# Kernel optimization log

Measured on AMD Instinct MI355X. Metric: run time of the kernel, lower is better.

Reference implementation:

```python
import jax, jax.numpy as jnp
import numpy as np

EMB = 256
HID = 1024
N_TRACKS = 4096
SEQ = 9
SCALE = 4.0


def setup_inputs() -> dict:
    key = jax.random.key(0)
    ks = jax.random.split(key, 12)

    def init(k, shape, fan_in):
        b = 1.0 / np.sqrt(fan_in)
        return jax.random.uniform(k, shape, jnp.float32, -b, b)

    return {
        "observed": jax.random.normal(ks[0], (SEQ, N_TRACKS, 2), jnp.float32),
        "emb_w": init(ks[1], (EMB - 2, 2), 2),
        "emb_b": init(ks[2], (EMB - 2,), 2),
        "enc_wih": init(ks[3], (4 * HID, EMB), HID),
        "enc_whh": init(ks[4], (4 * HID, HID), HID),
        "enc_b": init(ks[5], (4 * HID,), HID),
        "dec_wih": init(ks[6], (4 * HID, EMB), HID),
        "dec_whh": init(ks[7], (4 * HID, HID), HID),
        "dec_b": init(ks[8], (4 * HID,), HID),
        "h2n_w": init(ks[9], (5, HID), HID),
        "h2n_b": init(ks[10], (5,), HID),
        "n_predict": 12,
    }


def _forward(observed, emb_w, emb_b, enc_wih, enc_whh, enc_b,
             dec_wih, dec_whh, dec_b, h2n_w, h2n_b, n_predict):
    n = observed.shape[1]
    H = enc_whh.shape[1]
    E = enc_wih.shape[1]

    def cell(x, h, c, wih, whh, b):
        # PyTorch LSTMCell gate order: i, f, g, o
        g = x @ wih.T + h @ whh.T + b
        i, f, gg, o = jnp.split(g, 4, axis=-1)
        c = jax.nn.sigmoid(f) * c + jax.nn.sigmoid(i) * jnp.tanh(gg)
        h = jax.nn.sigmoid(o) * jnp.tanh(c)
        return h, c

    def embed(v):
        # Linear(2, E-2) -> ReLU, then 2 zero tag channels
        e = jax.nn.relu((v * SCALE) @ emb_w.T + emb_b)
        return jnp.concatenate([e, jnp.zeros((v.shape[0], 2), e.dtype)], axis=1)

    def h2n(h):
        raw = h @ h2n_w.T + h2n_b
        sig = 0.01 + 0.2 * jax.nn.sigmoid(raw[:, 2:4])  # sigma1, sigma2
        rho = 0.7 * jax.nn.sigmoid(raw[:, 4:5])          # rho
        return jnp.concatenate([raw[:, :2], sig, rho], axis=1)

    def step(params, h, c, obs1, obs2):
        wih, whh, b = params
        mask = ~(jnp.isnan(obs1[:, 0]) | jnp.isnan(obs2[:, 0]))  # [N]
        x = embed(obs2 - obs1)
        h2, c2 = cell(x, h, c, wih, whh, b)
        nrm = h2n(h2)
        m = mask[:, None]
        h = jnp.where(m, h2, h)
        c = jnp.where(m, c2, c)
        normal = jnp.where(m, nrm, jnp.nan)
        pos = obs2 + normal[:, :2]
        return h, c, normal, pos

    h = jnp.zeros((n, H), observed.dtype)
    c = jnp.zeros((n, H), observed.dtype)

    # encoder start tag
    tag_enc = jnp.zeros((n, E), observed.dtype).at[:, -2].set(1.0)
    h, c = cell(tag_enc, h, c, enc_wih, enc_whh, enc_b)

    enc_p = (enc_wih, enc_whh, enc_b)

    def enc_scan(carry, obs_pair):
        h, c = carry
        o1, o2 = obs_pair
        h, c, normal, pos = step(enc_p, h, c, o1, o2)
        return (h, c), (normal, pos)

    (h, c), (enc_normals, enc_positions) = jax.lax.scan(
        enc_scan, (h, c), (observed[:-1], observed[1:]))

    # decoder start tag
    tag_dec = jnp.zeros((n, E), observed.dtype).at[:, -1].set(1.0)
    h, c = cell(tag_dec, h, c, dec_wih, dec_whh, dec_b)

    dec_p = (dec_wih, dec_whh, dec_b)
    p1, p2 = enc_positions[-2], enc_positions[-1]

    def dec_scan(carry, _):
        h, c, p1, p2 = carry
        o1 = jax.lax.stop_gradient(p1)  # .detach() in torch
        o2 = jax.lax.stop_gradient(p2)
        h, c, normal, pos = step(dec_p, h, c, o1, o2)
        return (h, c, p2, pos), (normal, pos)

    _, (dec_normals, dec_positions) = jax.lax.scan(
        dec_scan, (h, c, p1, p2), None, length=n_predict - 1)

    rel_pred_scene = jnp.concatenate([enc_normals, dec_normals], axis=0)
    pred_scene = jnp.concatenate([enc_positions, dec_positions], axis=0)
    return rel_pred_scene, pred_scene


def reference(observed, emb_w, emb_b, enc_wih, enc_whh, enc_b,
              dec_wih, dec_whh, dec_b, h2n_w, h2n_b, n_predict):
    return _forward(observed, emb_w, emb_b, enc_wih, enc_whh, enc_b,
                    dec_wih, dec_whh, dec_b, h2n_w, h2n_b, n_predict)
```

## Files before the change

### kernel.cpp

```cpp
#include <hip/hip_runtime.h>
#include <stdint.h>

#define NTRK 4096
#define HIDN 1024
#define EMBN 256
#define KTOT 1280
#define NOUT 19

typedef __attribute__((ext_vector_type(8))) short short8;
typedef __attribute__((ext_vector_type(4))) float f32x4;

typedef __attribute__((address_space(1))) const void GV;
typedef __attribute__((address_space(3))) void LV;

__device__ __forceinline__ uint16_t f2bf(float f) {
  uint32_t u = __float_as_uint(f);
  u += 0x7fffu + ((u >> 16) & 1u);
  return (uint16_t)(u >> 16);
}
__device__ __forceinline__ float bf2f(uint16_t v) {
  return __uint_as_float(((uint32_t)v) << 16);
}
__device__ __forceinline__ float sigm(float x) { return 1.0f / (1.0f + expf(-x)); }
__device__ __forceinline__ float sigmf_(float x) {
  return __builtin_amdgcn_rcpf(1.0f + __expf(-x));
}
__device__ __forceinline__ float tanhf_(float x) {
  return 2.0f * __builtin_amdgcn_rcpf(1.0f + __expf(-2.0f * x)) - 1.0f;
}

__global__ __launch_bounds__(256) void prep_weights(
    const float* __restrict__ encWih, const float* __restrict__ encWhh,
    const float* __restrict__ encB,
    const float* __restrict__ decWih, const float* __restrict__ decWhh,
    const float* __restrict__ decB,
    uint16_t* __restrict__ WcatE, uint16_t* __restrict__ WcatD,
    float* __restrict__ biasE, float* __restrict__ biasD, float* __restrict__ biasDT)
{
  const int jp = blockIdx.x;
  const int q = jp >> 6, r = jp & 63;
  const int gate = r >> 4, l16 = r & 15;
  const int u = q * 16 + l16;
  const int orig = gate * 1024 + u;
  const int t = threadIdx.x;

  WcatE[(size_t)jp * KTOT + t] = f2bf(encWih[(size_t)orig * 256 + t]);
  WcatD[(size_t)jp * KTOT + t] = f2bf(decWih[(size_t)orig * 256 + t]);
#pragma unroll
  for (int c = 0; c < 4; c++) {
    WcatE[(size_t)jp * KTOT + 256 + c * 256 + t] = f2bf(encWhh[(size_t)orig * 1024 + c * 256 + t]);
    WcatD[(size_t)jp * KTOT + 256 + c * 256 + t] = f2bf(decWhh[(size_t)orig * 1024 + c * 256 + t]);
  }
  if (t == 0) {
    biasE[jp]  = encB[orig];
    biasD[jp]  = decB[orig];
    biasDT[jp] = decB[orig] + decWih[(size_t)orig * 256 + 255];
  }
}

__global__ void init_h0(const float* __restrict__ encWih, const float* __restrict__ encB,
                        float* __restrict__ h0, float* __restrict__ c0)
{
  const int u = blockIdx.x * 256 + threadIdx.x;
  if (u >= 1024) return;
  const float gi = encWih[(size_t)(u) * 256 + 254]        + encB[u];
  const float gg = encWih[(size_t)(2048 + u) * 256 + 254] + encB[2048 + u];
  const float go = encWih[(size_t)(3072 + u) * 256 + 254] + encB[3072 + u];
  const float c = sigm(gi) * tanhf(gg);
  c0[u] = c;
  h0[u] = sigm(go) * tanhf(c);
}

__global__ void fill_state(const float* __restrict__ h0, const float* __restrict__ c0,
                           uint16_t* __restrict__ H, float* __restrict__ Cst)
{
  const size_t i = (size_t)blockIdx.x * 256 + threadIdx.x;
  const int u = (int)(i & 1023);
  H[i] = f2bf(h0[u]);
  Cst[i] = c0[u];
}

__global__ __launch_bounds__(256) void embed_k(
    const float* __restrict__ o1, const float* __restrict__ o2,
    const float* __restrict__ ew, const float* __restrict__ eb,
    uint16_t* __restrict__ X)
{
  const int trk = blockIdx.x;
  const int j = threadIdx.x;
  const float vx = (o2[trk * 2]     - o1[trk * 2])     * 4.0f;
  const float vy = (o2[trk * 2 + 1] - o1[trk * 2 + 1]) * 4.0f;
  float e = 0.f;
  if (j < 254) e = fmaxf(vx * ew[j * 2] + vy * ew[j * 2 + 1] + eb[j], 0.f);
  X[(size_t)trk * 256 + j] = f2bf(e);
}

__global__ __launch_bounds__(256) void embed8(
    const float* __restrict__ observed, const float* __restrict__ ew,
    const float* __restrict__ eb, uint16_t* __restrict__ Xall)
{
  const int t = blockIdx.y;
  const int trk = blockIdx.x;
  const int j = threadIdx.x;
  const float* o1 = observed + ((size_t)t * 4096 + trk) * 2;
  const float* o2 = o1 + 4096 * 2;
  const float vx = (o2[0] - o1[0]) * 4.0f;
  const float vy = (o2[1] - o1[1]) * 4.0f;
  float e = 0.f;
  if (j < 254) e = fmaxf(vx * ew[j * 2] + vy * ew[j * 2 + 1] + eb[j], 0.f);
  Xall[((size_t)t * 4096 + trk) * 256 + j] = f2bf(e);
}

__global__ __launch_bounds__(512, 2) void gemm_lstm(
    const uint16_t* __restrict__ X,    const uint16_t* __restrict__ Hin,
    const uint16_t* __restrict__ Wcat, const float* __restrict__ bias,
    float* __restrict__ Cst,           uint16_t* __restrict__ Hout,
    const float* __restrict__ obs1,    const float* __restrict__ obs2,
    int k0, int maskmode)
{
  __shared__ uint16_t As[4 * 8192];
  __shared__ uint16_t Bs[4 * 8192];
  __shared__ uint16_t Dm[4096];
  __shared__ uint8_t  smask[256];

  const int tid  = threadIdx.x;
  const int w    = tid >> 6;
  const int lane = tid & 63;
  const int wr   = w >> 2;
  const int wc   = w & 3;
  const int quad = lane >> 4;
  const int l15  = lane & 15;

  const int bid = blockIdx.y * 16 + blockIdx.x;
  const int wg  = (bid & 7) * 32 + (bid >> 3);
  const int bm  = (wg >> 4) * 256;
  const int bn  = (wg & 15) * 256;

  const int NT = (KTOT - k0) >> 5;

  if (tid < 256) {
    bool m = true;
    if (maskmode) {
      const float a = obs1[(bm + tid) * 2];
      const float b = obs2[(bm + tid) * 2];
      m = !((a != a) || (b != b));
    }
    smask[tid] = m ? 1 : 0;
  }

  const int srow = w * 16 + (lane >> 2);
  const int kch  = (lane & 3) * 8;
  const uint16_t* pXa = X ? (X + (size_t)(bm + srow) * 256 + kch) : (const uint16_t*)0;
  const uint16_t* pHa = Hin  + (size_t)(bm + srow) * 1024 + kch;
  const uint16_t* pBa = Wcat + (size_t)(bn + srow) * (size_t)KTOT + kch;
  const int ldsw = w * 16 * 32;

  auto stage_tile = [&](int V) {
    if (V >= NT) {
      const GV* dsrc = (GV*)(Wcat + (size_t)tid * 8);
      LV* ddst = (LV*)(Dm + w * 512);
#pragma unroll
      for (int uu = 0; uu < 4; uu++)
        __builtin_amdgcn_global_load_lds(dsrc, ddst, 16, 0, 0);
      return;
    }
    const int kg = k0 + V * 32;
    uint16_t* asl = As + (V & 3) * 8192;
    uint16_t* bsl = Bs + (V & 3) * 8192;
    const uint16_t* a0;
    int rstride;
    if (kg < 256) { a0 = pXa + kg;         rstride = 256;  }
    else          { a0 = pHa + (kg - 256); rstride = 1024; }
    __builtin_amdgcn_global_load_lds((GV*)a0,                        (LV*)(asl + ldsw),        16, 0, 0);
    __builtin_amdgcn_global_load_lds((GV*)(a0 + 128 * rstride),      (LV*)(asl + 4096 + ldsw), 16, 0, 0);
    const uint16_t* b0 = pBa + kg;
    __builtin_amdgcn_global_load_lds((GV*)b0,                        (LV*)(bsl + ldsw),        16, 0, 0);
    __builtin_amdgcn_global_load_lds((GV*)(b0 + 128 * KTOT),         (LV*)(bsl + 4096 + ldsw), 16, 0, 0);
  };

  f32x4 acc[8][4];
#pragma unroll
  for (int i = 0; i < 8; i++)
#pragma unroll
    for (int j = 0; j < 4; j++) acc[i][j] = (f32x4){0.f, 0.f, 0.f, 0.f};

  stage_tile(0); stage_tile(1); stage_tile(2);
  asm volatile("s_waitcnt vmcnt(8)" ::: "memory");
  __builtin_amdgcn_s_barrier();

  const int aoff = (wr * 128 + l15) * 32 + quad * 8;
  const int boff = (wc * 64  + l15) * 32 + quad * 8;

  for (int T = 0; T < NT; ++T) {
    stage_tile(T + 3);
    const uint16_t* asl = As + (T & 3) * 8192;
    const uint16_t* bsl = Bs + (T & 3) * 8192;
    short8 bf[4], af[8];
#pragma unroll
    for (int n = 0; n < 4; n++)
      bf[n] = *(const short8*)(bsl + boff + n * 512);
#pragma unroll
    for (int m = 0; m < 8; m++)
      af[m] = *(const short8*)(asl + aoff + m * 512);
    __builtin_amdgcn_s_setprio(1);
#pragma unroll
    for (int m = 0; m < 8; m++)
#pragma unroll
      for (int n = 0; n < 4; n++)
        acc[m][n] = __builtin_amdgcn_mfma_f32_16x16x32_bf16(af[m], bf[n], acc[m][n], 0, 0, 0);
    __builtin_amdgcn_s_setprio(0);
    asm volatile("s_waitcnt lgkmcnt(0)" ::: "memory");
    __builtin_amdgcn_sched_barrier(0);
    asm volatile("s_waitcnt vmcnt(8)" ::: "memory");
    __builtin_amdgcn_s_barrier();
  }
  asm volatile("s_waitcnt vmcnt(0)" ::: "memory");

  const int u  = ((bn >> 6) + wc) * 16 + l15;
  const int jb = bn + wc * 64 + l15;
  const float b_i = bias[jb];
  const float b_f = bias[jb + 16];
  const float b_g = bias[jb + 32];
  const float b_o = bias[jb + 48];

#pragma unroll
  for (int mi = 0; mi < 8; mi++) {
#pragma unroll
    for (int r = 0; r < 4; r++) {
      const int row = bm + wr * 128 + mi * 16 + quad * 4 + r;
      const size_t idx = (size_t)row * 1024 + u;
      uint16_t hv;
      if (smask[row - bm]) {
        const float gi = acc[mi][0][r] + b_i;
        const float gf = acc[mi][1][r] + b_f;
        const float gg = acc[mi][2][r] + b_g;
        const float go = acc[mi][3][r] + b_o;
        const float cn = sigmf_(gf) * Cst[idx] + sigmf_(gi) * tanhf_(gg);
        Cst[idx] = cn;
        hv = f2bf(sigmf_(go) * tanhf_(cn));
      } else {
        hv = Hin[idx];
      }
      Hout[idx] = hv;
    }
  }
}

__global__ __launch_bounds__(256) void h2n_pos(
    const uint16_t* __restrict__ H, const float* __restrict__ w5, const float* __restrict__ b5,
    const float* __restrict__ obs1, const float* __restrict__ obs2,
    float* __restrict__ outrel, float* __restrict__ outpos,
    const float* __restrict__ pprev, const float* __restrict__ ew,
    const float* __restrict__ eb, uint16_t* __restrict__ Xnext, int do_embed)
{
  const int lane  = threadIdx.x & 63;
  const int track = blockIdx.x * 4 + (threadIdx.x >> 6);

  const uint16_t* hrow = H + (size_t)track * 1024 + lane * 16;
  const short8 v0 = *(const short8*)(hrow);
  const short8 v1 = *(const short8*)(hrow + 8);
  float hv[16];
#pragma unroll
  for (int j = 0; j < 8; j++) {
    hv[j]     = bf2f((uint16_t)v0[j]);
    hv[8 + j] = bf2f((uint16_t)v1[j]);
  }
  const int kb = lane * 16;
  float p[5];
#pragma unroll
  for (int o = 0; o < 5; o++) {
    const float* wr = w5 + (size_t)o * 1024 + kb;
    float s = 0.f;
#pragma unroll
    for (int j = 0; j < 16; j++) s += hv[j] * wr[j];
    p[o] = s;
  }
#pragma unroll
  for (int o = 0; o < 5; o++) {
    float v = p[o];
    v += __shfl_xor(v, 32); v += __shfl_xor(v, 16); v += __shfl_xor(v, 8);
    v += __shfl_xor(v, 4);  v += __shfl_xor(v, 2);  v += __shfl_xor(v, 1);
    p[o] = v;
  }
  const float o1x = obs1[track * 2];
  const float o2x = obs2[track * 2];
  const float o2y = obs2[track * 2 + 1];
  const bool msk = !((o1x != o1x) || (o2x != o2x));
  float n0 = p[0] + b5[0];
  float n1 = p[1] + b5[1];
  float n2 = 0.01f + 0.2f * sigmf_(p[2] + b5[2]);
  float n3 = 0.01f + 0.2f * sigmf_(p[3] + b5[3]);
  float n4 = 0.7f  * sigmf_(p[4] + b5[4]);
  if (!msk) {
    const float qn = __uint_as_float(0x7fc00000u);
    n0 = n1 = n2 = n3 = n4 = qn;
  }
  const float posx = o2x + n0;
  const float posy = o2y + n1;
  if (lane == 0) {
    float* rr = outrel + (size_t)track * 5;
    rr[0] = n0; rr[1] = n1; rr[2] = n2; rr[3] = n3; rr[4] = n4;
    outpos[track * 2]     = posx;
    outpos[track * 2 + 1] = posy;
  }
  if (do_embed) {
    const float vx = (posx - pprev[track * 2])     * 4.0f;
    const float vy = (posy - pprev[track * 2 + 1]) * 4.0f;
    uint16_t* xr = Xnext + (size_t)track * 256;
#pragma unroll
    for (int ii = 0; ii < 4; ii++) {
      const int j = ii * 64 + lane;
      float e = 0.f;
      if (j < 254) e = fmaxf(vx * ew[j * 2] + vy * ew[j * 2 + 1] + eb[j], 0.f);
      xr[j] = f2bf(e);
    }
  }
}

extern "C" void kernel_launch(void* const* d_in, const int* in_sizes, int n_in,
                              void* d_out, int out_size, void* d_ws, size_t ws_size,
                              hipStream_t stream)
{
  const float* observed = (const float*)d_in[0];
  const float* emb_w    = (const float*)d_in[1];
  const float* emb_b    = (const float*)d_in[2];
  const float* enc_wih  = (const float*)d_in[3];
  const float* enc_whh  = (const float*)d_in[4];
  const float* enc_b    = (const float*)d_in[5];
  const float* dec_wih  = (const float*)d_in[6];
  const float* dec_whh  = (const float*)d_in[7];
  const float* dec_b    = (const float*)d_in[8];
  const float* h2n_w    = (const float*)d_in[9];
  const float* h2n_b    = (const float*)d_in[10];

  char* ws = (char*)d_ws;
  size_t off = 0;
  auto alloc = [&](size_t bytes) -> void* {
    size_t cur = (off + 255) & ~(size_t)255;
    off = cur + bytes;
    return (void*)(ws + cur);
  };
  uint16_t* WcatE = (uint16_t*)alloc((size_t)4096 * KTOT * 2);
  uint16_t* WcatD = (uint16_t*)alloc((size_t)4096 * KTOT * 2);
  float*    biasE = (float*)alloc(4096 * 4);
  float*    biasD = (float*)alloc(4096 * 4);
  float*    biasDT= (float*)alloc(4096 * 4);
  float*    h0    = (float*)alloc(1024 * 4);
  float*    c0    = (float*)alloc(1024 * 4);
  uint16_t* HA    = (uint16_t*)alloc((size_t)4096 * 1024 * 2);
  uint16_t* HB    = (uint16_t*)alloc((size_t)4096 * 1024 * 2);
  float*    Cst   = (float*)alloc((size_t)4096 * 1024 * 4);
  uint16_t* Xb    = (uint16_t*)alloc((size_t)4096 * 256 * 2);
  const size_t xall_bytes = (size_t)8 * 4096 * 256 * 2;
  const bool use_xall = (off + 256 + xall_bytes) <= ws_size;
  uint16_t* Xall = use_xall ? (uint16_t*)alloc(xall_bytes) : nullptr;

  float* outrel = (float*)d_out;
  float* outpos = outrel + (size_t)NOUT * 4096 * 5;

  prep_weights<<<4096, 256, 0, stream>>>(enc_wih, enc_whh, enc_b, dec_wih, dec_whh, dec_b,
                                         WcatE, WcatD, biasE, biasD, biasDT);
  init_h0<<<4, 256, 0, stream>>>(enc_wih, enc_b, h0, c0);
  fill_state<<<16384, 256, 0, stream>>>(h0, c0, HA, Cst);
  if (use_xall) {
    embed8<<<dim3(4096, 8), 256, 0, stream>>>(observed, emb_w, emb_b, Xall);
  }

  uint16_t* Hin = HA;
  uint16_t* Hout = HB;
  const dim3 ggrid(16, 16);

  for (int t = 0; t < 8; t++) {
    const float* o1 = observed + (size_t)t * 4096 * 2;
    const float* o2 = observed + (size_t)(t + 1) * 4096 * 2;
    uint16_t* Xt = Xb;
    if (use_xall) {
      Xt = Xall + (size_t)t * 4096 * 256;
    } else {
      embed_k<<<4096, 256, 0, stream>>>(o1, o2, emb_w, emb_b, Xb);
    }
    gemm_lstm<<<ggrid, 512, 0, stream>>>(Xt, Hin, WcatE, biasE, Cst, Hout, o1, o2, 0, 1);
    const int de = (t == 7) ? 1 : 0;
    h2n_pos<<<1024, 256, 0, stream>>>(Hout, h2n_w, h2n_b, o1, o2,
                                      outrel + (size_t)t * 4096 * 5,
                                      outpos + (size_t)t * 4096 * 2,
                                      outpos + (size_t)6 * 4096 * 2, emb_w, emb_b, Xb, de);
    uint16_t* tmp = Hin; Hin = Hout; Hout = tmp;
  }

  gemm_lstm<<<ggrid, 512, 0, stream>>>(nullptr, Hin, WcatD, biasDT, Cst, Hout,
                                       nullptr, nullptr, 256, 0);
  { uint16_t* tmp = Hin; Hin = Hout; Hout = tmp; }

  for (int s = 0; s < 11; s++) {
    const float* p1 = outpos + (size_t)(6 + s) * 4096 * 2;
    const float* p2 = outpos + (size_t)(7 + s) * 4096 * 2;
    gemm_lstm<<<ggrid, 512, 0, stream>>>(Xb, Hin, WcatD, biasD, Cst, Hout, p1, p2, 0, 1);
    const int de = (s < 10) ? 1 : 0;
    h2n_pos<<<1024, 256, 0, stream>>>(Hout, h2n_w, h2n_b, p1, p2,
                                      outrel + (size_t)(8 + s) * 4096 * 5,
                                      outpos + (size_t)(8 + s) * 4096 * 2,
                                      p2, emb_w, emb_b, Xb, de);
    uint16_t* tmp = Hin; Hin = Hout; Hout = tmp;
  }
}
```

Before: 1.309 ms.

## Restructure LSTM GEMM mainloop into 64-wide K tiles with quadrant ping-pong staging

Replaces the 4-stage 32-wide K pipeline with a 2-stage double buffer of 64-wide K tiles. Each tile is split into four quadrant sub-steps, and each sub-step issues one part of the next tile's global-to-LDS loads before its MFMAs. LDS chunks are now XOR-swizzled to avoid bank conflicts on the wider rows. Wave-to-output mapping changes to 32x64 quadrants, and the epilogue is adjusted to match. This trades more barriers per K-step for better load/compute interleaving and fewer LDS conflicts, at the risk of a shallower prefetch depth.

```diff
diff --git a/kernel.cpp b/kernel.cpp
--- a/kernel.cpp
+++ b/kernel.cpp
@@ -117,25 +117,26 @@
     const float* __restrict__ obs1,    const float* __restrict__ obs2,
     int k0, int maskmode)
 {
-  __shared__ uint16_t As[4 * 8192];
-  __shared__ uint16_t Bs[4 * 8192];
-  __shared__ uint16_t Dm[4096];
+  __shared__ uint16_t As[2 * 16384];
+  __shared__ uint16_t Bs[2 * 16384];
+  __shared__ uint16_t Dm[512];
   __shared__ uint8_t  smask[256];
 
   const int tid  = threadIdx.x;
   const int w    = tid >> 6;
   const int lane = tid & 63;
-  const int wr   = w >> 2;
-  const int wc   = w & 3;
+  const int qr   = w & 3;
+  const int qc   = w >> 2;
   const int quad = lane >> 4;
   const int l15  = lane & 15;
+  const int e7   = l15 & 7;
 
   const int bid = blockIdx.y * 16 + blockIdx.x;
   const int wg  = (bid & 7) * 32 + (bid >> 3);
   const int bm  = (wg >> 4) * 256;
   const int bn  = (wg & 15) * 256;
 
-  const int NT = (KTOT - k0) >> 5;
+  const int NT = (KTOT - k0) >> 6;
 
   if (tid < 256) {
     bool m = true;
@@ -147,100 +148,172 @@
     smask[tid] = m ? 1 : 0;
   }
 
-  const int srow = w * 16 + (lane >> 2);
-  const int kch  = (lane & 3) * 8;
-  const uint16_t* pXa = X ? (X + (size_t)(bm + srow) * 256 + kch) : (const uint16_t*)0;
-  const uint16_t* pHa = Hin  + (size_t)(bm + srow) * 1024 + kch;
-  const uint16_t* pBa = Wcat + (size_t)(bn + srow) * (size_t)KTOT + kch;
-  const int ldsw = w * 16 * 32;
-
-  auto stage_tile = [&](int V) {
+  const int srow = w * 16 + (lane >> 3);
+  const int sch  = ((lane & 7) ^ (lane >> 3)) * 8;
+  const uint16_t* pXr = X ? X + (size_t)(bm + srow) * 256 + sch : (const uint16_t*)0;
+  const uint16_t* pHr = Hin  + (size_t)(bm + srow) * 1024 + sch;
+  const uint16_t* pWr = Wcat + (size_t)(bn + srow) * (size_t)KTOT + sch;
+
+  auto stage_half = [&](int V, int s) {
     if (V >= NT) {
       const GV* dsrc = (GV*)(Wcat + (size_t)tid * 8);
-      LV* ddst = (LV*)(Dm + w * 512);
-#pragma unroll
-      for (int uu = 0; uu < 4; uu++)
-        __builtin_amdgcn_global_load_lds(dsrc, ddst, 16, 0, 0);
+      __builtin_amdgcn_global_load_lds(dsrc, (LV*)Dm, 16, 0, 0);
+      __builtin_amdgcn_global_load_lds(dsrc, (LV*)Dm, 16, 0, 0);
       return;
     }
-    const int kg = k0 + V * 32;
-    uint16_t* asl = As + (V & 3) * 8192;
-    uint16_t* bsl = Bs + (V & 3) * 8192;
-    const uint16_t* a0;
-    int rstride;
-    if (kg < 256) { a0 = pXa + kg;         rstride = 256;  }
-    else          { a0 = pHa + (kg - 256); rstride = 1024; }
-    __builtin_amdgcn_global_load_lds((GV*)a0,                        (LV*)(asl + ldsw),        16, 0, 0);
-    __builtin_amdgcn_global_load_lds((GV*)(a0 + 128 * rstride),      (LV*)(asl + 4096 + ldsw), 16, 0, 0);
-    const uint16_t* b0 = pBa + kg;
-    __builtin_amdgcn_global_load_lds((GV*)b0,                        (LV*)(bsl + ldsw),        16, 0, 0);
-    __builtin_amdgcn_global_load_lds((GV*)(b0 + 128 * KTOT),         (LV*)(bsl + 4096 + ldsw), 16, 0, 0);
+    const int kg = k0 + V * 64;
+    const int h  = s >> 1;
+    const bool isA = !(s & 1);
+    uint16_t* dst = (isA ? As : Bs) + (V & 1) * 16384 + (h * 128 + w * 16) * 64;
+    if (isA) {
+      const bool inX = (kg < 256);
+      const uint16_t* src0 = inX ? (pXr + (size_t)(h * 128) * 256 + kg)
+                                 : (pHr + (size_t)(h * 128) * 1024 + (kg - 256));
+      const int rs = inX ? 256 : 1024;
+      __builtin_amdgcn_global_load_lds((GV*)src0,            (LV*)dst,            16, 0, 0);
+      __builtin_amdgcn_global_load_lds((GV*)(src0 + 8 * rs), (LV*)(dst + 8 * 64), 16, 0, 0);
+    } else {
+      const uint16_t* src0 = pWr + (size_t)(h * 128) * (size_t)KTOT + kg;
+      __builtin_amdgcn_global_load_lds((GV*)src0,              (LV*)dst,            16, 0, 0);
+      __builtin_amdgcn_global_load_lds((GV*)(src0 + 8 * KTOT), (LV*)(dst + 8 * 64), 16, 0, 0);
+    }
   };
 
-  f32x4 acc[8][4];
-#pragma unroll
-  for (int i = 0; i < 8; i++)
-#pragma unroll
-    for (int j = 0; j < 4; j++) acc[i][j] = (f32x4){0.f, 0.f, 0.f, 0.f};
-
-  stage_tile(0); stage_tile(1); stage_tile(2);
-  asm volatile("s_waitcnt vmcnt(8)" ::: "memory");
+  f32x4 acc[4][2][4];
+#pragma unroll
+  for (int p = 0; p < 4; p++)
+#pragma unroll
+    for (int i = 0; i < 2; i++)
+#pragma unroll
+      for (int n = 0; n < 4; n++) acc[p][i][n] = (f32x4){0.f, 0.f, 0.f, 0.f};
+
+  stage_half(0, 0); stage_half(0, 1); stage_half(0, 2); stage_half(0, 3);
+  asm volatile("s_waitcnt vmcnt(4)" ::: "memory");
   __builtin_amdgcn_s_barrier();
 
-  const int aoff = (wr * 128 + l15) * 32 + quad * 8;
-  const int boff = (wc * 64  + l15) * 32 + quad * 8;
-
-  for (int T = 0; T < NT; ++T) {
-    stage_tile(T + 3);
-    const uint16_t* asl = As + (T & 3) * 8192;
-    const uint16_t* bsl = Bs + (T & 3) * 8192;
-    short8 bf[4], af[8];
-#pragma unroll
-    for (int n = 0; n < 4; n++)
-      bf[n] = *(const short8*)(bsl + boff + n * 512);
-#pragma unroll
-    for (int m = 0; m < 8; m++)
-      af[m] = *(const short8*)(asl + aoff + m * 512);
-    __builtin_amdgcn_s_setprio(1);
-#pragma unroll
-    for (int m = 0; m < 8; m++)
-#pragma unroll
-      for (int n = 0; n < 4; n++)
-        acc[m][n] = __builtin_amdgcn_mfma_f32_16x16x32_bf16(af[m], bf[n], acc[m][n], 0, 0, 0);
-    __builtin_amdgcn_s_setprio(0);
+  const int arow = (qr * 32 + l15) * 64;
+  const int brow = (qc * 64 + l15) * 64;
+  const int cc0  = (quad ^ e7) * 8;
+  const int cc1  = ((4 + quad) ^ e7) * 8;
+
+  for (int T = 0; T < NT; T++) {
+    const uint16_t* Ab = As + (T & 1) * 16384;
+    const uint16_t* Bb = Bs + (T & 1) * 16384;
+    short8 a0[2][2], a1[2][2], bf[4][2];
+
+#pragma unroll
+    for (int i = 0; i < 2; i++) {
+      a0[i][0] = *(const short8*)(Ab + arow + i * 1024 + cc0);
+      a0[i][1] = *(const short8*)(Ab + arow + i * 1024 + cc1);
+    }
+#pragma unroll
+    for (int n = 0; n < 4; n++) {
+      bf[n][0] = *(const short8*)(Bb + brow + n * 1024 + cc0);
+      bf[n][1] = *(const short8*)(Bb + brow + n * 1024 + cc1);
+    }
+    stage_half(T + 1, 0);
+    __builtin_amdgcn_s_barrier();
     asm volatile("s_waitcnt lgkmcnt(0)" ::: "memory");
     __builtin_amdgcn_sched_barrier(0);
-    asm volatile("s_waitcnt vmcnt(8)" ::: "memory");
+    __builtin_amdgcn_s_setprio(1);
+#pragma unroll
+    for (int i = 0; i < 2; i++)
+#pragma unroll
+      for (int n = 0; n < 4; n++) {
+        acc[0][i][n] = __builtin_amdgcn_mfma_f32_16x16x32_bf16(a0[i][0], bf[n][0], acc[0][i][n], 0, 0, 0);
+        acc[0][i][n] = __builtin_amdgcn_mfma_f32_16x16x32_bf16(a0[i][1], bf[n][1], acc[0][i][n], 0, 0, 0);
+      }
+    __builtin_amdgcn_s_setprio(0);
+    asm volatile("s_waitcnt vmcnt(4)" ::: "memory");
+    __builtin_amdgcn_s_barrier();
+
+#pragma unroll
+    for (int i = 0; i < 2; i++) {
+      a1[i][0] = *(const short8*)(Ab + 8192 + arow + i * 1024 + cc0);
+      a1[i][1] = *(const short8*)(Ab + 8192 + arow + i * 1024 + cc1);
+    }
+    stage_half(T + 1, 1);
+    __builtin_amdgcn_s_barrier();
+    asm volatile("s_waitcnt lgkmcnt(0)" ::: "memory");
+    __builtin_amdgcn_sched_barrier(0);
+    __builtin_amdgcn_s_setprio(1);
+#pragma unroll
+    for (int i = 0; i < 2; i++)
+#pragma unroll
+      for (int n = 0; n < 4; n++) {
+        acc[1][i][n] = __builtin_amdgcn_mfma_f32_16x16x32_bf16(a1[i][0], bf[n][0], acc[1][i][n], 0, 0, 0);
+        acc[1][i][n] = __builtin_amdgcn_mfma_f32_16x16x32_bf16(a1[i][1], bf[n][1], acc[1][i][n], 0, 0, 0);
+      }
+    __builtin_amdgcn_s_setprio(0);
+    asm volatile("s_waitcnt vmcnt(4)" ::: "memory");
+    __builtin_amdgcn_s_barrier();
+
+#pragma unroll
+    for (int n = 0; n < 4; n++) {
+      bf[n][0] = *(const short8*)(Bb + 8192 + brow + n * 1024 + cc0);
+      bf[n][1] = *(const short8*)(Bb + 8192 + brow + n * 1024 + cc1);
+    }
+    stage_half(T + 1, 2);
+    __builtin_amdgcn_s_barrier();
+    asm volatile("s_waitcnt lgkmcnt(0)" ::: "memory");
+    __builtin_amdgcn_sched_barrier(0);
+    __builtin_amdgcn_s_setprio(1);
+#pragma unroll
+    for (int i = 0; i < 2; i++)
+#pragma unroll
+      for (int n = 0; n < 4; n++) {
+        acc[2][i][n] = __builtin_amdgcn_mfma_f32_16x16x32_bf16(a1[i][0], bf[n][0], acc[2][i][n], 0, 0, 0);
+        acc[2][i][n] = __builtin_amdgcn_mfma_f32_16x16x32_bf16(a1[i][1], bf[n][1], acc[2][i][n], 0, 0, 0);
+      }
+    __builtin_amdgcn_s_setprio(0);
+    __builtin_amdgcn_s_barrier();
+
+    stage_half(T + 1, 3);
+    __builtin_amdgcn_s_barrier();
+    __builtin_amdgcn_s_setprio(1);
+#pragma unroll
+    for (int i = 0; i < 2; i++)
+#pragma unroll
+      for (int n = 0; n < 4; n++) {
+        acc[3][i][n] = __builtin_amdgcn_mfma_f32_16x16x32_bf16(a0[i][0], bf[n][0], acc[3][i][n], 0, 0, 0);
+        acc[3][i][n] = __builtin_amdgcn_mfma_f32_16x16x32_bf16(a0[i][1], bf[n][1], acc[3][i][n], 0, 0, 0);
+      }
+    __builtin_amdgcn_s_setprio(0);
+    asm volatile("s_waitcnt vmcnt(4)" ::: "memory");
     __builtin_amdgcn_s_barrier();
   }
   asm volatile("s_waitcnt vmcnt(0)" ::: "memory");
 
-  const int u  = ((bn >> 6) + wc) * 16 + l15;
-  const int jb = bn + wc * 64 + l15;
-  const float b_i = bias[jb];
-  const float b_f = bias[jb + 16];
-  const float b_g = bias[jb + 32];
-  const float b_o = bias[jb + 48];
-
-#pragma unroll
-  for (int mi = 0; mi < 8; mi++) {
-#pragma unroll
-    for (int r = 0; r < 4; r++) {
-      const int row = bm + wr * 128 + mi * 16 + quad * 4 + r;
-      const size_t idx = (size_t)row * 1024 + u;
-      uint16_t hv;
-      if (smask[row - bm]) {
-        const float gi = acc[mi][0][r] + b_i;
-        const float gf = acc[mi][1][r] + b_f;
-        const float gg = acc[mi][2][r] + b_g;
-        const float go = acc[mi][3][r] + b_o;
-        const float cn = sigmf_(gf) * Cst[idx] + sigmf_(gi) * tanhf_(gg);
-        Cst[idx] = cn;
-        hv = f2bf(sigmf_(go) * tanhf_(cn));
-      } else {
-        hv = Hin[idx];
+#pragma unroll
+  for (int p = 0; p < 4; p++) {
+    const int ah = (p == 1 || p == 2) ? 1 : 0;
+    const int bh = p >> 1;
+    const int u  = ((bn >> 6) + bh * 2 + qc) * 16 + l15;
+    const int jb = bn + bh * 128 + qc * 64 + l15;
+    const float b_i = bias[jb];
+    const float b_f = bias[jb + 16];
+    const float b_g = bias[jb + 32];
+    const float b_o = bias[jb + 48];
+#pragma unroll
+    for (int i = 0; i < 2; i++) {
+#pragma unroll
+      for (int r = 0; r < 4; r++) {
+        const int row = bm + ah * 128 + qr * 32 + i * 16 + quad * 4 + r;
+        const size_t idx = (size_t)row * 1024 + u;
+        uint16_t hv;
+        if (smask[row - bm]) {
+          const float gi = acc[p][i][0][r] + b_i;
+          const float gf = acc[p][i][1][r] + b_f;
+          const float gg = acc[p][i][2][r] + b_g;
+          const float go = acc[p][i][3][r] + b_o;
+          const float cn = sigmf_(gf) * Cst[idx] + sigmf_(gi) * tanhf_(gg);
+          Cst[idx] = cn;
+          hv = f2bf(sigmf_(go) * tanhf_(cn));
+        } else {
+          hv = Hin[idx];
+        }
+        Hout[idx] = hv;
       }
-      Hout[idx] = hv;
     }
   }
 }
```

After: 1.312 ms. Within noise of the previous version (+0.3%).

## Shrink LSTM GEMM tile to 128x256 with swizzled LDS and triple buffering

Applied to the files above, without the earlier changes.

Halves the M tile of the fused LSTM GEMM from 256 to 128 rows, doubling the grid to 512 blocks, and cuts the accumulator set per wave to 4x4. LDS buffering drops from four stages to three, the dummy-load padding is removed, and an XOR swizzle is applied to LDS chunk placement to reduce bank conflicts. Block-to-tile mapping is changed so each XCD group covers a contiguous M/N region for L2 reuse. The aim is higher occupancy (launch bounds 512,4) and better latency hiding, at the cost of more weight traffic per output and less arithmetic intensity per tile.

```diff
diff --git a/kernel.cpp b/kernel.cpp
--- a/kernel.cpp
+++ b/kernel.cpp
@@ -110,17 +110,16 @@
   Xall[((size_t)t * 4096 + trk) * 256 + j] = f2bf(e);
 }
 
-__global__ __launch_bounds__(512, 2) void gemm_lstm(
+__global__ __launch_bounds__(512, 4) void gemm_lstm(
     const uint16_t* __restrict__ X,    const uint16_t* __restrict__ Hin,
     const uint16_t* __restrict__ Wcat, const float* __restrict__ bias,
     float* __restrict__ Cst,           uint16_t* __restrict__ Hout,
     const float* __restrict__ obs1,    const float* __restrict__ obs2,
     int k0, int maskmode)
 {
-  __shared__ uint16_t As[4 * 8192];
-  __shared__ uint16_t Bs[4 * 8192];
-  __shared__ uint16_t Dm[4096];
-  __shared__ uint8_t  smask[256];
+  __shared__ uint16_t As[3 * 4096];
+  __shared__ uint16_t Bs[3 * 8192];
+  __shared__ uint8_t  smask[128];
 
   const int tid  = threadIdx.x;
   const int w    = tid >> 6;
@@ -131,13 +130,16 @@
   const int l15  = lane & 15;
 
   const int bid = blockIdx.y * 16 + blockIdx.x;
-  const int wg  = (bid & 7) * 32 + (bid >> 3);
-  const int bm  = (wg >> 4) * 256;
-  const int bn  = (wg & 15) * 256;
+  const int xcd = bid & 7;
+  const int j   = bid >> 3;
+  const int bmS = (xcd >> 2) * 16 + (j >> 2);
+  const int bnS = (xcd & 3) * 4 + (j & 3);
+  const int bm  = bmS * 128;
+  const int bn  = bnS * 256;
 
   const int NT = (KTOT - k0) >> 5;
 
-  if (tid < 256) {
+  if (tid < 128) {
     bool m = true;
     if (maskmode) {
       const float a = obs1[(bm + tid) * 2];
@@ -148,72 +150,65 @@
   }
 
   const int srow = w * 16 + (lane >> 2);
-  const int kch  = (lane & 3) * 8;
-  const uint16_t* pXa = X ? (X + (size_t)(bm + srow) * 256 + kch) : (const uint16_t*)0;
-  const uint16_t* pHa = Hin  + (size_t)(bm + srow) * 1024 + kch;
-  const uint16_t* pBa = Wcat + (size_t)(bn + srow) * (size_t)KTOT + kch;
-  const int ldsw = w * 16 * 32;
-
-  auto stage_tile = [&](int V) {
-    if (V >= NT) {
-      const GV* dsrc = (GV*)(Wcat + (size_t)tid * 8);
-      LV* ddst = (LV*)(Dm + w * 512);
-#pragma unroll
-      for (int uu = 0; uu < 4; uu++)
-        __builtin_amdgcn_global_load_lds(dsrc, ddst, 16, 0, 0);
-      return;
-    }
+  const int sch  = ((lane & 3) ^ ((lane >> 3) & 3)) * 8;
+  const uint16_t* pXr = X ? X + (size_t)(bm + srow) * 256 + sch : (const uint16_t*)0;
+  const uint16_t* pHr = Hin  + (size_t)(bm + srow) * 1024 + sch;
+  const uint16_t* pWr = Wcat + (size_t)(bn + srow) * (size_t)KTOT + sch;
+
+  auto stage = [&](int V, int slot) {
+    if (V >= NT) return;
     const int kg = k0 + V * 32;
-    uint16_t* asl = As + (V & 3) * 8192;
-    uint16_t* bsl = Bs + (V & 3) * 8192;
-    const uint16_t* a0;
-    int rstride;
-    if (kg < 256) { a0 = pXa + kg;         rstride = 256;  }
-    else          { a0 = pHa + (kg - 256); rstride = 1024; }
-    __builtin_amdgcn_global_load_lds((GV*)a0,                        (LV*)(asl + ldsw),        16, 0, 0);
-    __builtin_amdgcn_global_load_lds((GV*)(a0 + 128 * rstride),      (LV*)(asl + 4096 + ldsw), 16, 0, 0);
-    const uint16_t* b0 = pBa + kg;
-    __builtin_amdgcn_global_load_lds((GV*)b0,                        (LV*)(bsl + ldsw),        16, 0, 0);
-    __builtin_amdgcn_global_load_lds((GV*)(b0 + 128 * KTOT),         (LV*)(bsl + 4096 + ldsw), 16, 0, 0);
+    uint16_t* ad = As + slot * 4096 + w * 16 * 32;
+    if (kg < 256) {
+      __builtin_amdgcn_global_load_lds((GV*)(pXr + kg),         (LV*)ad, 16, 0, 0);
+    } else {
+      __builtin_amdgcn_global_load_lds((GV*)(pHr + (kg - 256)), (LV*)ad, 16, 0, 0);
+    }
+    uint16_t* bd = Bs + slot * 8192 + w * 16 * 32;
+    __builtin_amdgcn_global_load_lds((GV*)(pWr + kg),                        (LV*)bd,          16, 0, 0);
+    __builtin_amdgcn_global_load_lds((GV*)(pWr + (size_t)128 * KTOT + kg),   (LV*)(bd + 4096), 16, 0, 0);
   };
 
-  f32x4 acc[8][4];
-#pragma unroll
-  for (int i = 0; i < 8; i++)
-#pragma unroll
-    for (int j = 0; j < 4; j++) acc[i][j] = (f32x4){0.f, 0.f, 0.f, 0.f};
-
-  stage_tile(0); stage_tile(1); stage_tile(2);
-  asm volatile("s_waitcnt vmcnt(8)" ::: "memory");
+  f32x4 acc[4][4];
+#pragma unroll
+  for (int i = 0; i < 4; i++)
+#pragma unroll
+    for (int n = 0; n < 4; n++) acc[i][n] = (f32x4){0.f, 0.f, 0.f, 0.f};
+
+  stage(0, 0); stage(1, 1);
+  asm volatile("s_waitcnt vmcnt(3)" ::: "memory");
   __builtin_amdgcn_s_barrier();
 
-  const int aoff = (wr * 128 + l15) * 32 + quad * 8;
-  const int boff = (wc * 64  + l15) * 32 + quad * 8;
-
-  for (int T = 0; T < NT; ++T) {
-    stage_tile(T + 3);
-    const uint16_t* asl = As + (T & 3) * 8192;
-    const uint16_t* bsl = Bs + (T & 3) * 8192;
-    short8 bf[4], af[8];
+  const int cc = (quad ^ ((l15 >> 1) & 3)) * 8;
+
+  int sT = 0;
+  for (int T = 0; T < NT; T++) {
+    const int sS = (sT == 0) ? 2 : sT - 1;
+    const uint16_t* Ab = As + sT * 4096;
+    const uint16_t* Bb = Bs + sT * 8192;
+    short8 a[4], b[4];
+#pragma unroll
+    for (int i = 0; i < 4; i++)
+      a[i] = *(const short8*)(Ab + (wr * 64 + i * 16 + l15) * 32 + cc);
 #pragma unroll
     for (int n = 0; n < 4; n++)
-      bf[n] = *(const short8*)(bsl + boff + n * 512);
-#pragma unroll
-    for (int m = 0; m < 8; m++)
-      af[m] = *(const short8*)(asl + aoff + m * 512);
+      b[n] = *(const short8*)(Bb + (wc * 64 + n * 16 + l15) * 32 + cc);
+    stage(T + 2, sS);
     __builtin_amdgcn_s_setprio(1);
 #pragma unroll
-    for (int m = 0; m < 8; m++)
+    for (int i = 0; i < 4; i++)
 #pragma unroll
       for (int n = 0; n < 4; n++)
-        acc[m][n] = __builtin_amdgcn_mfma_f32_16x16x32_bf16(af[m], bf[n], acc[m][n], 0, 0, 0);
+        acc[i][n] = __builtin_amdgcn_mfma_f32_16x16x32_bf16(a[i], b[n], acc[i][n], 0, 0, 0);
     __builtin_amdgcn_s_setprio(0);
-    asm volatile("s_waitcnt lgkmcnt(0)" ::: "memory");
-    __builtin_amdgcn_sched_barrier(0);
-    asm volatile("s_waitcnt vmcnt(8)" ::: "memory");
+    if (T < NT - 2) {
+      asm volatile("s_waitcnt vmcnt(3)" ::: "memory");
+    } else {
+      asm volatile("s_waitcnt vmcnt(0)" ::: "memory");
+    }
     __builtin_amdgcn_s_barrier();
-  }
-  asm volatile("s_waitcnt vmcnt(0)" ::: "memory");
+    sT = (sT == 2) ? 0 : sT + 1;
+  }
 
   const int u  = ((bn >> 6) + wc) * 16 + l15;
   const int jb = bn + wc * 64 + l15;
@@ -223,17 +218,17 @@
   const float b_o = bias[jb + 48];
 
 #pragma unroll
-  for (int mi = 0; mi < 8; mi++) {
+  for (int i = 0; i < 4; i++) {
 #pragma unroll
     for (int r = 0; r < 4; r++) {
-      const int row = bm + wr * 128 + mi * 16 + quad * 4 + r;
+      const int row = bm + wr * 64 + i * 16 + quad * 4 + r;
       const size_t idx = (size_t)row * 1024 + u;
       uint16_t hv;
       if (smask[row - bm]) {
-        const float gi = acc[mi][0][r] + b_i;
-        const float gf = acc[mi][1][r] + b_f;
-        const float gg = acc[mi][2][r] + b_g;
-        const float go = acc[mi][3][r] + b_o;
+        const float gi = acc[i][0][r] + b_i;
+        const float gf = acc[i][1][r] + b_f;
+        const float gg = acc[i][2][r] + b_g;
+        const float go = acc[i][3][r] + b_o;
         const float cn = sigmf_(gf) * Cst[idx] + sigmf_(gi) * tanhf_(gg);
         Cst[idx] = cn;
         hv = f2bf(sigmf_(go) * tanhf_(cn));
@@ -367,7 +362,7 @@
 
   uint16_t* Hin = HA;
   uint16_t* Hout = HB;
-  const dim3 ggrid(16, 16);
+  const dim3 ggrid(16, 32);
 
   for (int t = 0; t < 8; t++) {
     const float* o1 = observed + (size_t)t * 4096 * 2;
```

After: 1.257 ms. 1.04x faster.
